# Kernel optimization log

Hardware: AMD Instinct MI355X
Metric: run time of the kernel (lower is better)

## Reference

```python
import jax, jax.numpy as jnp
import numpy as np

B, N, V = 8, 2000, 2000
K = 100            # local_size
EMB = 128          # ff_hidden_dim
PENALTY = -1e9
EPS = 1e-5         # InstanceNorm eps


def setup_inputs() -> dict:
    key = jax.random.key(0)
    ks = jax.random.split(key, 16)
    s = 0.02
    return {
        "dist": jax.random.uniform(ks[0], (B, N, V), dtype=jnp.float32),
        "theta": jax.random.normal(ks[1], (B, N, V), dtype=jnp.float32),
        "scale": jax.random.uniform(ks[2], (B, N, 1), dtype=jnp.float32),
        # Linear params stored [in, out]
        "w1": jax.random.normal(ks[3], (2 * K + 1, EMB), dtype=jnp.float32) * s,
        "b1": jnp.zeros((EMB,), jnp.float32),
        "w2": jax.random.normal(ks[4], (EMB, 2 * EMB), dtype=jnp.float32) * s,
        "b2": jnp.zeros((2 * EMB,), jnp.float32),
        "w3": jax.random.normal(ks[5], (2 * EMB, EMB), dtype=jnp.float32) * s,
        "b3": jnp.zeros((EMB,), jnp.float32),
        "w4": jax.random.normal(ks[6], (EMB, K), dtype=jnp.float32) * s,
        "b4": jnp.zeros((K,), jnp.float32),
        "gamma": jnp.ones((2 * EMB,), jnp.float32),   # InstanceNorm affine weight
        "beta": jnp.zeros((2 * EMB,), jnp.float32),   # InstanceNorm affine bias
    }


def reference(dist, theta, scale, w1, b1, w2, b2, w3, b3, w4, b4, gamma, beta):
    # --- topk smallest distances (ascending) + gather theta ---
    neg_vals, idx = jax.lax.top_k(-dist, K)          # [B,N,K]
    sorted_dist = -neg_vals                           # ascending k smallest
    sorted_dist = sorted_dist / jnp.max(sorted_dist, axis=-1, keepdims=True)
    sorted_theta = jnp.take_along_axis(theta, idx, axis=-1)  # [B,N,K]

    # --- small MLP with InstanceNorm over the node dim ---
    x_in = jnp.concatenate([sorted_dist, sorted_theta, scale], axis=-1)  # [B,N,2K+1]
    emb = jax.nn.relu(x_in @ w1 + b1)                 # [B,N,EMB]
    h = jax.nn.relu(emb @ w2 + b2)                    # [B,N,2*EMB]
    # InstanceNorm1d: normalize each channel over the length (node) dim, biased var
    mean = jnp.mean(h, axis=1, keepdims=True)
    var = jnp.var(h, axis=1, keepdims=True)
    h = (h - mean) * jax.lax.rsqrt(var + EPS) * gamma + beta
    emb = jax.nn.relu(h @ w3 + b3)                    # [B,N,EMB]
    out = (emb @ w4 + b4) - sorted_dist               # [B,N,K]

    # --- scatter into penalty-initialized matrix ---
    out_mat = jnp.full((B, N, V), PENALTY, dtype=dist.dtype)
    b_ix = jnp.arange(B)[:, None, None]
    n_ix = jnp.arange(N)[None, :, None]
    return out_mat.at[b_ix, n_ix, idx].set(out)
```

## Files before the change

### kernel.cpp

```cpp
#include <hip/hip_runtime.h>
#include <hip/hip_bf16.h>

#define BB 8
#define NN 2000
#define VV 2000
#define KK 100
#define EMB 128
#define PENALTY -1e9f
#define NBIN 512
#define BINSCALE 2048.0f
#define CAP 200
#define XPAD 224

typedef __attribute__((ext_vector_type(8))) short short8;
typedef __attribute__((ext_vector_type(4))) float f32x4;

__device__ __forceinline__ unsigned short bf16rne(float f) {
    unsigned u = __float_as_uint(f);
    u += 0x7FFF + ((u >> 16) & 1);
    return (unsigned short)(u >> 16);
}
__device__ __forceinline__ float bf2f(unsigned short s) {
    return __uint_as_float((unsigned)s << 16);
}

__global__ __launch_bounds__(256) void wpack_kernel(
    const float* __restrict__ w1, const float* __restrict__ w2,
    const float* __restrict__ w3, const float* __restrict__ w4,
    unsigned short* __restrict__ pw1, unsigned short* __restrict__ pw2,
    unsigned short* __restrict__ pw3, unsigned short* __restrict__ pw4)
{
    const int bt = blockIdx.x;
    const int t = threadIdx.x;
    for (int e = t; e < 512; e += 256) {
        int lane = e >> 3, j = e & 7;
        int kk = ((lane >> 4) << 3) + j;
        int nn = lane & 15;
        if (bt < 56) {
            int kt = bt >> 3, nt = bt & 7;
            int k = kt * 32 + kk, n = nt * 16 + nn;
            float f = (k < 201) ? w1[k * 128 + n] : 0.f;
            pw1[bt * 512 + e] = bf16rne(f);
        } else if (bt < 120) {
            int bb = bt - 56, kt = bb >> 4, nt = bb & 15;
            pw2[bb * 512 + e] = bf16rne(w2[(kt * 32 + kk) * 256 + nt * 16 + nn]);
        } else if (bt < 184) {
            int bb = bt - 120, kt = bb >> 3, nt = bb & 7;
            pw3[bb * 512 + e] = bf16rne(w3[(kt * 32 + kk) * 128 + nt * 16 + nn]);
        } else {
            int bb = bt - 184, kt = bb / 7, nt = bb % 7;
            int n = nt * 16 + nn;
            float f = (n < 100) ? w4[(kt * 32 + kk) * 100 + n] : 0.f;
            pw4[bb * 512 + e] = bf16rne(f);
        }
    }
}

__global__ __launch_bounds__(256) void topk_kernel(
    const float* __restrict__ dist, const float* __restrict__ theta,
    const float* __restrict__ scale,
    unsigned short* __restrict__ xin, float* __restrict__ sdist,
    int* __restrict__ idxb)
{
    __shared__ __align__(16) unsigned hist[NBIN];
    __shared__ unsigned long long comp[CAP];
    __shared__ unsigned wsum[4];
    __shared__ int sh_Bt, sh_m, sh_mult;
    __shared__ int sh_cnt, sh_ntie, sh_kth;
    __shared__ unsigned sh_pref;
    __shared__ int sh_tie[64];
    __shared__ float sh_Tf;

    const int row = blockIdx.x;
    const int t = threadIdx.x;
    const int lane = t & 63, wid = t >> 6;
    const float* drow = dist + (size_t)row * VV;

    unsigned kb[8];
    int bn[8];
    if (t < VV / 8) {
        const float4* d4 = (const float4*)drow;
        float4 a = d4[t * 2], b2 = d4[t * 2 + 1];
        float vv[8] = {a.x, a.y, a.z, a.w, b2.x, b2.y, b2.z, b2.w};
#pragma unroll
        for (int j = 0; j < 8; ++j) {
            kb[j] = __float_as_uint(vv[j]);
            int b = (int)(vv[j] * BINSCALE);
            bn[j] = b < 0 ? 0 : (b > NBIN - 1 ? NBIN - 1 : b);
        }
    } else {
#pragma unroll
        for (int j = 0; j < 8; ++j) { kb[j] = 0xFFFFFFFFu; bn[j] = NBIN - 1; }
    }

    hist[t] = 0u;
    hist[t + 256] = 0u;
    if (t == 0) { sh_cnt = 0; sh_ntie = 0; sh_mult = 1; sh_Bt = NBIN - 1; sh_m = 100000; }
    __syncthreads();
#pragma unroll
    for (int j = 0; j < 8; ++j)
        if (bn[j] < NBIN - 1) atomicAdd(&hist[bn[j]], 1u);
    __syncthreads();

    uint2 cc = *(const uint2*)&hist[2 * t];
    const unsigned c0 = cc.x, c1 = cc.y;
    const unsigned tot = c0 + c1;
    unsigned incl = tot;
#pragma unroll
    for (int off = 1; off < 64; off <<= 1) {
        unsigned v = __shfl_up(incl, (unsigned)off);
        if (lane >= off) incl += v;
    }
    if (lane == 63) wsum[wid] = incl;
    __syncthreads();
    unsigned woff = 0;
    for (int w = 0; w < wid; ++w) woff += wsum[w];
    const unsigned excl = woff + incl - tot;
    const unsigned run = excl + tot;

    { uint2 off2; off2.x = excl; off2.y = excl + c0; *(uint2*)&hist[2 * t] = off2; }
    if (excl < KK && excl + c0 >= KK) {
        sh_Bt = 2 * t; sh_m = (int)(excl + c0);
    } else if (t < 255 && excl + c0 < KK && run >= KK) {
        sh_Bt = 2 * t + 1; sh_m = (int)run;
    }
    __syncthreads();
    const int Bt = sh_Bt;
    const int m = sh_m;

    {
        int mx = 0;
        if (2 * t <= Bt) mx = (int)c0;
        if (2 * t + 1 <= Bt) mx = mx > (int)c1 ? mx : (int)c1;
        if (mx > 1) atomicMax(&sh_mult, mx);
    }

    if (m <= CAP) {
#pragma unroll
        for (int j = 0; j < 8; ++j) {
            if (bn[j] <= Bt) {
                int slot = (int)atomicAdd(&hist[bn[j]], 1u);
                comp[slot] = ((unsigned long long)kb[j] << 32) | (unsigned)(t * 8 + j);
            }
        }
        __syncthreads();
        const int passes = (sh_mult > 1) ? sh_mult + 1 : 0;
        for (int p = 0; p < passes; ++p) {
            int i = 2 * t + (p & 1);
            if (i + 1 < m) {
                unsigned long long a = comp[i], b2 = comp[i + 1];
                if (a > b2) { comp[i] = b2; comp[i + 1] = a; }
            }
            __syncthreads();
        }
        const float Tf = __uint_as_float((unsigned)(comp[KK - 1] >> 32));
        const float invT = 1.0f / Tf;
        const float* trow = theta + (size_t)row * VV;
        if (t < KK) {
            unsigned long long c = comp[t];
            unsigned kbits = (unsigned)(c >> 32);
            int id = (int)(c & 0xFFFFFFFFu);
            float nv = __uint_as_float(kbits) * invT;
            xin[(size_t)row * XPAD + t] = bf16rne(nv);
            xin[(size_t)row * XPAD + 100 + t] = bf16rne(trow[id]);
            sdist[(size_t)row * KK + t] = nv;
            idxb[(size_t)row * KK + t] = id;
        }
        if (t == 255) xin[(size_t)row * XPAD + 200] = bf16rne(scale[row]);
    } else {
#pragma unroll
        for (int j = 0; j < 8; ++j) {
            if (bn[j] < Bt) {
                int pos = atomicAdd(&sh_cnt, 1);
                if (pos < CAP)
                    comp[pos] = ((unsigned long long)kb[j] << 32) | (unsigned)(t * 8 + j);
            }
        }
        __syncthreads();
        int nless = sh_cnt;
        if (t == 0) { sh_pref = 0u; sh_kth = KK - nless; }
        __syncthreads();
        for (int p = 0; p < 4; ++p) {
            if (t < 256) hist[t] = 0u;
            __syncthreads();
            const int shift = 24 - 8 * p;
            const unsigned pref = sh_pref;
#pragma unroll
            for (int j = 0; j < 8; ++j) {
                if (bn[j] == Bt) {
                    unsigned k = kb[j];
                    bool ok = (p == 0) || ((k >> (shift + 8)) == pref);
                    if (ok) atomicAdd(&hist[(k >> shift) & 255u], 1u);
                }
            }
            __syncthreads();
            if (t == 0) {
                int kth = sh_kth;
                unsigned cum = 0;
                int b = 0;
                for (; b < 256; ++b) {
                    unsigned c = hist[b];
                    if (cum + c >= (unsigned)kth) break;
                    cum += c;
                }
                sh_pref = (pref << 8) | (unsigned)b;
                sh_kth = kth - (int)cum;
            }
            __syncthreads();
        }
        const unsigned T = sh_pref;
        const int need2 = sh_kth;
#pragma unroll
        for (int j = 0; j < 8; ++j) {
            if (bn[j] == Bt) {
                unsigned k = kb[j];
                if (k < T) {
                    int pos = atomicAdd(&sh_cnt, 1);
                    if (pos < CAP)
                        comp[pos] = ((unsigned long long)k << 32) | (unsigned)(t * 8 + j);
                } else if (k == T) {
                    int q = atomicAdd(&sh_ntie, 1);
                    if (q < 64) sh_tie[q] = t * 8 + j;
                }
            }
        }
        __syncthreads();
        if (t == 0) {
            int nl2 = sh_cnt;
            int nt = sh_ntie < 64 ? sh_ntie : 64;
            for (int i = 1; i < nt; ++i) {
                int v = sh_tie[i], j2 = i - 1;
                while (j2 >= 0 && sh_tie[j2] > v) { sh_tie[j2 + 1] = sh_tie[j2]; --j2; }
                sh_tie[j2 + 1] = v;
            }
            for (int i = 0; i < need2; ++i)
                comp[nl2 + i] = ((unsigned long long)T << 32) | (unsigned)sh_tie[i];
            sh_cnt = nl2 + need2;
        }
        __syncthreads();
        const int mm = sh_cnt;
        unsigned long long c = (t < mm) ? comp[t] : ~0ull;
        int rank = 0;
        if (t < mm) {
            for (int j = 0; j < mm; ++j) {
                unsigned long long cj = comp[j];
                rank += (cj < c) || (cj == c && j < t);
            }
            if (rank == KK - 1) sh_Tf = __uint_as_float((unsigned)(c >> 32));
        }
        __syncthreads();
        const float invT = 1.0f / sh_Tf;
        const float* trow = theta + (size_t)row * VV;
        if (t < mm && rank < KK) {
            unsigned kbits = (unsigned)(c >> 32);
            int id = (int)(c & 0xFFFFFFFFu);
            float nv = __uint_as_float(kbits) * invT;
            xin[(size_t)row * XPAD + rank] = bf16rne(nv);
            xin[(size_t)row * XPAD + 100 + rank] = bf16rne(trow[id]);
            sdist[(size_t)row * KK + rank] = nv;
            idxb[(size_t)row * KK + rank] = id;
        }
        if (t == 255) xin[(size_t)row * XPAD + 200] = bf16rne(scale[row]);
    }
}

__global__ __launch_bounds__(256) void fused12_mfma(
    const unsigned short* __restrict__ xin, const unsigned short* __restrict__ pw1,
    const float* __restrict__ b1, const unsigned short* __restrict__ pw2,
    const float* __restrict__ b2, unsigned short* __restrict__ h)
{
    __shared__ unsigned short c1s[64][136];
    const int t = threadIdx.x;
    const int w = t >> 6, l = t & 63;
    const int m0 = blockIdx.x * 64;
    const int lr = l & 15, lg = l >> 4;

    f32x4 acc[8] = {};
    const short8* arow = (const short8*)(xin + (size_t)(m0 + 16 * w + lr) * XPAD);
    const short8* pw1v = (const short8*)pw1;
#pragma unroll
    for (int kt = 0; kt < 7; ++kt) {
        short8 a = arow[kt * 4 + lg];
#pragma unroll
        for (int nt = 0; nt < 8; ++nt) {
            short8 b = pw1v[(kt * 8 + nt) * 64 + l];
            acc[nt] = __builtin_amdgcn_mfma_f32_16x16x32_bf16(a, b, acc[nt], 0, 0, 0);
        }
    }
#pragma unroll
    for (int nt = 0; nt < 8; ++nt) {
        int col = nt * 16 + lr;
        float bb = b1[col];
#pragma unroll
        for (int r = 0; r < 4; ++r) {
            float v = fmaxf(acc[nt][r] + bb, 0.f);
            c1s[16 * w + lg * 4 + r][col] = bf16rne(v);
        }
    }
    __syncthreads();

    f32x4 acc2[16] = {};
    const short8* pw2v = (const short8*)pw2;
#pragma unroll
    for (int kt = 0; kt < 4; ++kt) {
        short8 a = *(const short8*)&c1s[16 * w + lr][kt * 32 + lg * 8];
#pragma unroll
        for (int nt = 0; nt < 16; ++nt) {
            short8 b = pw2v[(kt * 16 + nt) * 64 + l];
            acc2[nt] = __builtin_amdgcn_mfma_f32_16x16x32_bf16(a, b, acc2[nt], 0, 0, 0);
        }
    }
#pragma unroll
    for (int nt = 0; nt < 16; ++nt) {
        int col = nt * 16 + lr;
        float bb = b2[col];
#pragma unroll
        for (int r = 0; r < 4; ++r) {
            float v = fmaxf(acc2[nt][r] + bb, 0.f);
            h[(size_t)(m0 + 16 * w + lg * 4 + r) * 256 + col] = bf16rne(v);
        }
    }
}

#define NCHUNK 25
#define CHUNK (NN / NCHUNK)

__global__ __launch_bounds__(256) void stats_partial(
    const unsigned short* __restrict__ h, float* __restrict__ part)
{
    const int b = blockIdx.x, ch = blockIdx.y, c = threadIdx.x;
    const unsigned short* base = h + ((size_t)b * NN + (size_t)ch * CHUNK) * 256 + c;
    float s = 0.f, s2 = 0.f;
    for (int n = 0; n < CHUNK; ++n) {
        float v = bf2f(base[(size_t)n * 256]);
        s += v;
        s2 += v * v;
    }
    size_t o = (((size_t)b * NCHUNK + ch) * 256 + c) * 2;
    part[o] = s;
    part[o + 1] = s2;
}

__global__ __launch_bounds__(256) void stats_final(
    const float* __restrict__ part, const float* __restrict__ gamma,
    const float* __restrict__ beta, float* __restrict__ scv,
    float* __restrict__ shv)
{
    const int b = blockIdx.x, c = threadIdx.x;
    float s = 0.f, s2 = 0.f;
    for (int ch = 0; ch < NCHUNK; ++ch) {
        size_t o = (((size_t)b * NCHUNK + ch) * 256 + c) * 2;
        s += part[o];
        s2 += part[o + 1];
    }
    const float inv = 1.0f / (float)NN;
    float mean = s * inv;
    float var = s2 * inv - mean * mean;
    float rs = rsqrtf(var + 1e-5f);
    float sc = gamma[c] * rs;
    scv[b * 256 + c] = sc;
    shv[b * 256 + c] = beta[c] - mean * sc;
}

__global__ __launch_bounds__(256) void fused34_mfma(
    const unsigned short* __restrict__ h, const unsigned short* __restrict__ pw3,
    const float* __restrict__ b3, const unsigned short* __restrict__ pw4,
    const float* __restrict__ b4, const float* __restrict__ scv,
    const float* __restrict__ shv, const float* __restrict__ sdist,
    const int* __restrict__ idxb, float* __restrict__ out)
{
    __shared__ unsigned short c1s[64][136];
    const int t = threadIdx.x;
    const int w = t >> 6, l = t & 63;
    const int m0 = blockIdx.x * 64;
    const int lr = l & 15, lg = l >> 4;

    {
        float4* o4 = (float4*)(out + (size_t)m0 * VV);
        const float4 pv = make_float4(PENALTY, PENALTY, PENALTY, PENALTY);
        for (int i = t; i < 64 * VV / 4; i += 256) o4[i] = pv;
    }

    const int myrow = m0 + 16 * w + lr;
    const int mybatch = myrow / NN;

    f32x4 acc[8] = {};
    const short8* hrow = (const short8*)(h + (size_t)myrow * 256);
    const short8* pw3v = (const short8*)pw3;
#pragma unroll
    for (int kt = 0; kt < 8; ++kt) {
        int k0 = kt * 32 + lg * 8;
        short8 hv = hrow[kt * 4 + lg];
        const float4* scp = (const float4*)(scv + mybatch * 256 + k0);
        const float4* shp = (const float4*)(shv + mybatch * 256 + k0);
        float4 sc0 = scp[0], sc1 = scp[1];
        float4 sh0 = shp[0], sh1 = shp[1];
        short8 a;
        a[0] = (short)bf16rne(fmaf(bf2f((unsigned short)hv[0]), sc0.x, sh0.x));
        a[1] = (short)bf16rne(fmaf(bf2f((unsigned short)hv[1]), sc0.y, sh0.y));
        a[2] = (short)bf16rne(fmaf(bf2f((unsigned short)hv[2]), sc0.z, sh0.z));
        a[3] = (short)bf16rne(fmaf(bf2f((unsigned short)hv[3]), sc0.w, sh0.w));
        a[4] = (short)bf16rne(fmaf(bf2f((unsigned short)hv[4]), sc1.x, sh1.x));
        a[5] = (short)bf16rne(fmaf(bf2f((unsigned short)hv[5]), sc1.y, sh1.y));
        a[6] = (short)bf16rne(fmaf(bf2f((unsigned short)hv[6]), sc1.z, sh1.z));
        a[7] = (short)bf16rne(fmaf(bf2f((unsigned short)hv[7]), sc1.w, sh1.w));
#pragma unroll
        for (int nt = 0; nt < 8; ++nt) {
            short8 b = pw3v[(kt * 8 + nt) * 64 + l];
            acc[nt] = __builtin_amdgcn_mfma_f32_16x16x32_bf16(a, b, acc[nt], 0, 0, 0);
        }
    }
#pragma unroll
    for (int nt = 0; nt < 8; ++nt) {
        int col = nt * 16 + lr;
        float bb = b3[col];
#pragma unroll
        for (int r = 0; r < 4; ++r) {
            float v = fmaxf(acc[nt][r] + bb, 0.f);
            c1s[16 * w + lg * 4 + r][col] = bf16rne(v);
        }
    }
    __syncthreads();

    f32x4 acc2[7] = {};
    const short8* pw4v = (const short8*)pw4;
#pragma unroll
    for (int kt = 0; kt < 4; ++kt) {
        short8 a = *(const short8*)&c1s[16 * w + lr][kt * 32 + lg * 8];
#pragma unroll
        for (int nt = 0; nt < 7; ++nt) {
            short8 b = pw4v[(kt * 7 + nt) * 64 + l];
            acc2[nt] = __builtin_amdgcn_mfma_f32_16x16x32_bf16(a, b, acc2[nt], 0, 0, 0);
        }
    }
#pragma unroll
    for (int nt = 0; nt < 7; ++nt) {
        int col = nt * 16 + lr;
        if (col < KK) {
            float bb = b4[col];
#pragma unroll
            for (int r = 0; r < 4; ++r) {
                int mrow = m0 + 16 * w + lg * 4 + r;
                float v = acc2[nt][r] + bb - sdist[(size_t)mrow * KK + col];
                int id = idxb[(size_t)mrow * KK + col];
                out[(size_t)mrow * VV + id] = v;
            }
        }
    }
}

extern "C" void kernel_launch(void* const* d_in, const int* in_sizes, int n_in,
                              void* d_out, int out_size, void* d_ws, size_t ws_size,
                              hipStream_t stream)
{
    const float* dist  = (const float*)d_in[0];
    const float* theta = (const float*)d_in[1];
    const float* scale = (const float*)d_in[2];
    const float* w1 = (const float*)d_in[3];
    const float* b1 = (const float*)d_in[4];
    const float* w2 = (const float*)d_in[5];
    const float* b2 = (const float*)d_in[6];
    const float* w3 = (const float*)d_in[7];
    const float* b3 = (const float*)d_in[8];
    const float* w4 = (const float*)d_in[9];
    const float* b4 = (const float*)d_in[10];
    const float* gamma = (const float*)d_in[11];
    const float* beta  = (const float*)d_in[12];
    float* out = (float*)d_out;

    const int M = BB * NN;

    char* p = (char*)d_ws;
    unsigned short* xin = (unsigned short*)p;       p += (size_t)M * XPAD * 2;
    unsigned short* h   = (unsigned short*)p;       p += (size_t)M * 256 * 2;
    float* sdist = (float*)p;                       p += (size_t)M * KK * 4;
    int*   idxb  = (int*)p;                         p += (size_t)M * KK * 4;
    float* part  = (float*)p;                       p += (size_t)BB * NCHUNK * 256 * 2 * 4;
    float* scv   = (float*)p;                       p += 8 * 256 * 4;
    float* shv   = (float*)p;                       p += 8 * 256 * 4;
    unsigned short* pw1 = (unsigned short*)p;       p += 56 * 512 * 2;
    unsigned short* pw2 = (unsigned short*)p;       p += 64 * 512 * 2;
    unsigned short* pw3 = (unsigned short*)p;       p += 64 * 512 * 2;
    unsigned short* pw4 = (unsigned short*)p;       p += 28 * 512 * 2;

    wpack_kernel<<<212, 256, 0, stream>>>(w1, w2, w3, w4, pw1, pw2, pw3, pw4);

    topk_kernel<<<M, 256, 0, stream>>>(dist, theta, scale, xin, sdist, idxb);

    fused12_mfma<<<M / 64, 256, 0, stream>>>(xin, pw1, b1, pw2, b2, h);

    stats_partial<<<dim3(BB, NCHUNK), 256, 0, stream>>>(h, part);
    stats_final<<<BB, 256, 0, stream>>>(part, gamma, beta, scv, shv);

    fused34_mfma<<<M / 64, 256, 0, stream>>>(h, pw3, b3, pw4, b4, scv, shv,
                                             sdist, idxb, out);
}
```

Baseline: 140.9 us.

## Move penalty fill into topk, rank-sort within bins, split theta gather out

Three changes. The penalty fill of the output moves from the final MLP kernel into the top-k kernel, where it can overlap with the dist loads that kernel is memory-bound on. The odd-even transposition sort over bins is replaced by a per-element rank count within each bin, followed by a scatter, which removes the sort's many barrier passes. The theta gather moves out of the top-k kernel into a separate gather kernel, which adds a launch and extra reads of idxb.

```diff
diff --git a/kernel.cpp b/kernel.cpp
--- a/kernel.cpp
+++ b/kernel.cpp
@@ -57,15 +57,15 @@
 }
 
 __global__ __launch_bounds__(256) void topk_kernel(
-    const float* __restrict__ dist, const float* __restrict__ theta,
-    const float* __restrict__ scale,
+    const float* __restrict__ dist, const float* __restrict__ scale,
     unsigned short* __restrict__ xin, float* __restrict__ sdist,
-    int* __restrict__ idxb)
+    int* __restrict__ idxb, float* __restrict__ out)
 {
     __shared__ __align__(16) unsigned hist[NBIN];
+    __shared__ __align__(16) unsigned binstart[NBIN];
     __shared__ unsigned long long comp[CAP];
     __shared__ unsigned wsum[4];
-    __shared__ int sh_Bt, sh_m, sh_mult;
+    __shared__ int sh_Bt, sh_m;
     __shared__ int sh_cnt, sh_ntie, sh_kth;
     __shared__ unsigned sh_pref;
     __shared__ int sh_tie[64];
@@ -76,11 +76,24 @@
     const int lane = t & 63, wid = t >> 6;
     const float* drow = dist + (size_t)row * VV;
 
+    float4 a, b2;
+    const bool live = (t < VV / 8);
+    if (live) {
+        const float4* d4 = (const float4*)drow;
+        a = d4[t * 2];
+        b2 = d4[t * 2 + 1];
+    }
+
+    {
+        float4* orow4 = (float4*)(out + (size_t)row * VV);
+        const float4 pv = make_float4(PENALTY, PENALTY, PENALTY, PENALTY);
+        orow4[t] = pv;
+        if (t + 256 < VV / 4) orow4[t + 256] = pv;
+    }
+
     unsigned kb[8];
     int bn[8];
-    if (t < VV / 8) {
-        const float4* d4 = (const float4*)drow;
-        float4 a = d4[t * 2], b2 = d4[t * 2 + 1];
+    if (live) {
         float vv[8] = {a.x, a.y, a.z, a.w, b2.x, b2.y, b2.z, b2.w};
 #pragma unroll
         for (int j = 0; j < 8; ++j) {
@@ -95,7 +108,7 @@
 
     hist[t] = 0u;
     hist[t + 256] = 0u;
-    if (t == 0) { sh_cnt = 0; sh_ntie = 0; sh_mult = 1; sh_Bt = NBIN - 1; sh_m = 100000; }
+    if (t == 0) { sh_cnt = 0; sh_ntie = 0; sh_Bt = NBIN - 1; sh_m = 100000; }
     __syncthreads();
 #pragma unroll
     for (int j = 0; j < 8; ++j)
@@ -118,7 +131,11 @@
     const unsigned excl = woff + incl - tot;
     const unsigned run = excl + tot;
 
-    { uint2 off2; off2.x = excl; off2.y = excl + c0; *(uint2*)&hist[2 * t] = off2; }
+    {
+        uint2 st; st.x = excl; st.y = excl + c0;
+        *(uint2*)&hist[2 * t] = st;
+        *(uint2*)&binstart[2 * t] = st;
+    }
     if (excl < KK && excl + c0 >= KK) {
         sh_Bt = 2 * t; sh_m = (int)(excl + c0);
     } else if (t < 255 && excl + c0 < KK && run >= KK) {
@@ -128,41 +145,44 @@
     const int Bt = sh_Bt;
     const int m = sh_m;
 
-    {
-        int mx = 0;
-        if (2 * t <= Bt) mx = (int)c0;
-        if (2 * t + 1 <= Bt) mx = mx > (int)c1 ? mx : (int)c1;
-        if (mx > 1) atomicMax(&sh_mult, mx);
-    }
-
     if (m <= CAP) {
+        bool win[8];
 #pragma unroll
         for (int j = 0; j < 8; ++j) {
-            if (bn[j] <= Bt) {
+            win[j] = (bn[j] <= Bt);
+            if (win[j]) {
                 int slot = (int)atomicAdd(&hist[bn[j]], 1u);
                 comp[slot] = ((unsigned long long)kb[j] << 32) | (unsigned)(t * 8 + j);
             }
         }
         __syncthreads();
-        const int passes = (sh_mult > 1) ? sh_mult + 1 : 0;
-        for (int p = 0; p < passes; ++p) {
-            int i = 2 * t + (p & 1);
-            if (i + 1 < m) {
-                unsigned long long a = comp[i], b2 = comp[i + 1];
-                if (a > b2) { comp[i] = b2; comp[i + 1] = a; }
-            }
-            __syncthreads();
-        }
+        int rk[8];
+#pragma unroll
+        for (int j = 0; j < 8; ++j) {
+            if (win[j]) {
+                unsigned long long key =
+                    ((unsigned long long)kb[j] << 32) | (unsigned)(t * 8 + j);
+                unsigned s0 = binstart[bn[j]];
+                unsigned e0 = hist[bn[j]];
+                int r = (int)s0;
+                for (unsigned s = s0; s < e0; ++s) r += (comp[s] < key);
+                rk[j] = r;
+            }
+        }
+        __syncthreads();
+#pragma unroll
+        for (int j = 0; j < 8; ++j)
+            if (win[j])
+                comp[rk[j]] = ((unsigned long long)kb[j] << 32) | (unsigned)(t * 8 + j);
+        __syncthreads();
         const float Tf = __uint_as_float((unsigned)(comp[KK - 1] >> 32));
         const float invT = 1.0f / Tf;
-        const float* trow = theta + (size_t)row * VV;
         if (t < KK) {
             unsigned long long c = comp[t];
             unsigned kbits = (unsigned)(c >> 32);
             int id = (int)(c & 0xFFFFFFFFu);
             float nv = __uint_as_float(kbits) * invT;
             xin[(size_t)row * XPAD + t] = bf16rne(nv);
-            xin[(size_t)row * XPAD + 100 + t] = bf16rne(trow[id]);
             sdist[(size_t)row * KK + t] = nv;
             idxb[(size_t)row * KK + t] = id;
         }
@@ -250,18 +270,28 @@
         }
         __syncthreads();
         const float invT = 1.0f / sh_Tf;
-        const float* trow = theta + (size_t)row * VV;
         if (t < mm && rank < KK) {
             unsigned kbits = (unsigned)(c >> 32);
             int id = (int)(c & 0xFFFFFFFFu);
             float nv = __uint_as_float(kbits) * invT;
             xin[(size_t)row * XPAD + rank] = bf16rne(nv);
-            xin[(size_t)row * XPAD + 100 + rank] = bf16rne(trow[id]);
             sdist[(size_t)row * KK + rank] = nv;
             idxb[(size_t)row * KK + rank] = id;
         }
         if (t == 255) xin[(size_t)row * XPAD + 200] = bf16rne(scale[row]);
     }
+}
+
+__global__ __launch_bounds__(256) void gather_kernel(
+    const float* __restrict__ theta, const int* __restrict__ idxb,
+    unsigned short* __restrict__ xin)
+{
+    const int i = blockIdx.x * 256 + threadIdx.x;
+    const int row = i / KK;
+    const int k = i - row * KK;
+    const int id = idxb[i];
+    float v = theta[(size_t)row * VV + id];
+    xin[(size_t)row * XPAD + 100 + k] = bf16rne(v);
 }
 
 __global__ __launch_bounds__(256) void fused12_mfma(
@@ -374,12 +404,6 @@
     const int w = t >> 6, l = t & 63;
     const int m0 = blockIdx.x * 64;
     const int lr = l & 15, lg = l >> 4;
-
-    {
-        float4* o4 = (float4*)(out + (size_t)m0 * VV);
-        const float4 pv = make_float4(PENALTY, PENALTY, PENALTY, PENALTY);
-        for (int i = t; i < 64 * VV / 4; i += 256) o4[i] = pv;
-    }
 
     const int myrow = m0 + 16 * w + lr;
     const int mybatch = myrow / NN;
@@ -485,7 +509,9 @@
 
     wpack_kernel<<<212, 256, 0, stream>>>(w1, w2, w3, w4, pw1, pw2, pw3, pw4);
 
-    topk_kernel<<<M, 256, 0, stream>>>(dist, theta, scale, xin, sdist, idxb);
+    topk_kernel<<<M, 256, 0, stream>>>(dist, scale, xin, sdist, idxb, out);
+
+    gather_kernel<<<(M * KK) / 256, 256, 0, stream>>>(theta, idxb, xin);
 
     fused12_mfma<<<M / 64, 256, 0, stream>>>(xin, pw1, b1, pw2, b2, h);
 
```

After: 144.8 us. 2.7% more time.

## Process one top-k row per wavefront and split theta gather into separate kernel

Applied to the files above, without the earlier changes.

The top-k kernel now gives each 64-lane wavefront its own row, with four rows per block. All block-wide __syncthreads are replaced by wave barriers and per-wave shared arrays. The odd-even transposition sort of candidates is replaced by a per-bin rank computation that scatters into a second buffer. The theta gather moves into a separate elementwise kernel to spread the random reads across more threads. The aim is to remove block synchronisation overhead and serial sort passes, at the cost of more shared memory per block, an extra launch, and a round-trip of idx through global memory.

```diff
diff --git a/kernel.cpp b/kernel.cpp
--- a/kernel.cpp
+++ b/kernel.cpp
@@ -15,6 +15,8 @@
 typedef __attribute__((ext_vector_type(8))) short short8;
 typedef __attribute__((ext_vector_type(4))) float f32x4;
 
+#define WB() __builtin_amdgcn_wave_barrier()
+
 __device__ __forceinline__ unsigned short bf16rne(float f) {
     unsigned u = __float_as_uint(f);
     u += 0x7FFF + ((u >> 16) & 1);
@@ -23,6 +25,14 @@
 __device__ __forceinline__ float bf2f(unsigned short s) {
     return __uint_as_float((unsigned)s << 16);
 }
+
+#define FORALL_VALS(BODY)                                                    \
+    _Pragma("unroll") for (int c = 0; c < 8; ++c) {                          \
+        { const float fv = v4[c].x; const int e = (c * 64 + lane) * 4 + 0; BODY } \
+        { const float fv = v4[c].y; const int e = (c * 64 + lane) * 4 + 1; BODY } \
+        { const float fv = v4[c].z; const int e = (c * 64 + lane) * 4 + 2; BODY } \
+        { const float fv = v4[c].w; const int e = (c * 64 + lane) * 4 + 3; BODY } \
+    }
 
 __global__ __launch_bounds__(256) void wpack_kernel(
     const float* __restrict__ w1, const float* __restrict__ w2,
@@ -57,211 +67,232 @@
 }
 
 __global__ __launch_bounds__(256) void topk_kernel(
-    const float* __restrict__ dist, const float* __restrict__ theta,
-    const float* __restrict__ scale,
+    const float* __restrict__ dist, const float* __restrict__ scale,
     unsigned short* __restrict__ xin, float* __restrict__ sdist,
     int* __restrict__ idxb)
 {
-    __shared__ __align__(16) unsigned hist[NBIN];
-    __shared__ unsigned long long comp[CAP];
-    __shared__ unsigned wsum[4];
-    __shared__ int sh_Bt, sh_m, sh_mult;
-    __shared__ int sh_cnt, sh_ntie, sh_kth;
-    __shared__ unsigned sh_pref;
-    __shared__ int sh_tie[64];
-    __shared__ float sh_Tf;
-
-    const int row = blockIdx.x;
+    __shared__ __align__(16) unsigned hist[4][NBIN];
+    __shared__ __align__(16) unsigned binstart[4][NBIN];
+    __shared__ unsigned long long comp[4][CAP];
+    __shared__ unsigned long long comp2[4][CAP];
+    __shared__ int sh_cnt[4], sh_ntie[4], sh_kth[4];
+    __shared__ unsigned sh_pref[4];
+    __shared__ int sh_tie[4][64];
+
     const int t = threadIdx.x;
-    const int lane = t & 63, wid = t >> 6;
-    const float* drow = dist + (size_t)row * VV;
-
-    unsigned kb[8];
-    int bn[8];
-    if (t < VV / 8) {
-        const float4* d4 = (const float4*)drow;
-        float4 a = d4[t * 2], b2 = d4[t * 2 + 1];
-        float vv[8] = {a.x, a.y, a.z, a.w, b2.x, b2.y, b2.z, b2.w};
-#pragma unroll
-        for (int j = 0; j < 8; ++j) {
-            kb[j] = __float_as_uint(vv[j]);
-            int b = (int)(vv[j] * BINSCALE);
-            bn[j] = b < 0 ? 0 : (b > NBIN - 1 ? NBIN - 1 : b);
-        }
-    } else {
-#pragma unroll
-        for (int j = 0; j < 8; ++j) { kb[j] = 0xFFFFFFFFu; bn[j] = NBIN - 1; }
-    }
-
-    hist[t] = 0u;
-    hist[t + 256] = 0u;
-    if (t == 0) { sh_cnt = 0; sh_ntie = 0; sh_mult = 1; sh_Bt = NBIN - 1; sh_m = 100000; }
-    __syncthreads();
-#pragma unroll
-    for (int j = 0; j < 8; ++j)
-        if (bn[j] < NBIN - 1) atomicAdd(&hist[bn[j]], 1u);
-    __syncthreads();
-
-    uint2 cc = *(const uint2*)&hist[2 * t];
-    const unsigned c0 = cc.x, c1 = cc.y;
-    const unsigned tot = c0 + c1;
+    const int w = t >> 6, lane = t & 63;
+    const int row = blockIdx.x * 4 + w;
+    const float4* d4 = (const float4*)(dist + (size_t)row * VV);
+
+    float4 v4[8];
+#pragma unroll
+    for (int c = 0; c < 7; ++c) v4[c] = d4[c * 64 + lane];
+    v4[7] = (lane < 52) ? d4[448 + lane] : make_float4(2.f, 2.f, 2.f, 2.f);
+
+    {
+        uint4 z = make_uint4(0u, 0u, 0u, 0u);
+        *(uint4*)&hist[w][lane * 8] = z;
+        *(uint4*)&hist[w][lane * 8 + 4] = z;
+    }
+    if (lane == 0) { sh_cnt[w] = 0; sh_ntie[w] = 0; }
+    WB();
+
+    FORALL_VALS({
+        int b = (int)(fv * BINSCALE);
+        b = b < 0 ? 0 : b;
+        if (b < NBIN - 1) atomicAdd(&hist[w][b], 1u);
+        (void)e;
+    });
+    WB();
+
+    uint4 h0 = *(const uint4*)&hist[w][lane * 8];
+    uint4 h1 = *(const uint4*)&hist[w][lane * 8 + 4];
+    unsigned c8[8] = {h0.x, h0.y, h0.z, h0.w, h1.x, h1.y, h1.z, h1.w};
+    unsigned tot = 0;
+#pragma unroll
+    for (int b = 0; b < 8; ++b) tot += c8[b];
     unsigned incl = tot;
 #pragma unroll
     for (int off = 1; off < 64; off <<= 1) {
         unsigned v = __shfl_up(incl, (unsigned)off);
         if (lane >= off) incl += v;
     }
-    if (lane == 63) wsum[wid] = incl;
-    __syncthreads();
-    unsigned woff = 0;
-    for (int w = 0; w < wid; ++w) woff += wsum[w];
-    const unsigned excl = woff + incl - tot;
-    const unsigned run = excl + tot;
-
-    { uint2 off2; off2.x = excl; off2.y = excl + c0; *(uint2*)&hist[2 * t] = off2; }
-    if (excl < KK && excl + c0 >= KK) {
-        sh_Bt = 2 * t; sh_m = (int)(excl + c0);
-    } else if (t < 255 && excl + c0 < KK && run >= KK) {
-        sh_Bt = 2 * t + 1; sh_m = (int)run;
-    }
-    __syncthreads();
-    const int Bt = sh_Bt;
-    const int m = sh_m;
-
+    const unsigned excl = incl - tot;
+
+    int myBt = -1, myM = 0;
     {
-        int mx = 0;
-        if (2 * t <= Bt) mx = (int)c0;
-        if (2 * t + 1 <= Bt) mx = mx > (int)c1 ? mx : (int)c1;
-        if (mx > 1) atomicMax(&sh_mult, mx);
+        unsigned runv = excl;
+        unsigned st[8];
+#pragma unroll
+        for (int b = 0; b < 8; ++b) {
+            st[b] = runv;
+            if (myBt < 0 && runv < KK && runv + c8[b] >= KK) {
+                myBt = lane * 8 + b;
+                myM = (int)(runv + c8[b]);
+            }
+            runv += c8[b];
+        }
+        uint4 s0 = make_uint4(st[0], st[1], st[2], st[3]);
+        uint4 s1 = make_uint4(st[4], st[5], st[6], st[7]);
+        *(uint4*)&hist[w][lane * 8] = s0;
+        *(uint4*)&hist[w][lane * 8 + 4] = s1;
+        *(uint4*)&binstart[w][lane * 8] = s0;
+        *(uint4*)&binstart[w][lane * 8 + 4] = s1;
+    }
+    WB();
+
+    unsigned long long bl = __ballot(myBt >= 0);
+    int Bt, m;
+    if (bl != 0ull) {
+        int src = __ffsll(bl) - 1;
+        Bt = __shfl(myBt, src);
+        m = __shfl(myM, src);
+    } else {
+        Bt = NBIN - 1;
+        m = 100000;
     }
 
     if (m <= CAP) {
-#pragma unroll
-        for (int j = 0; j < 8; ++j) {
-            if (bn[j] <= Bt) {
-                int slot = (int)atomicAdd(&hist[bn[j]], 1u);
-                comp[slot] = ((unsigned long long)kb[j] << 32) | (unsigned)(t * 8 + j);
-            }
-        }
-        __syncthreads();
-        const int passes = (sh_mult > 1) ? sh_mult + 1 : 0;
-        for (int p = 0; p < passes; ++p) {
-            int i = 2 * t + (p & 1);
-            if (i + 1 < m) {
-                unsigned long long a = comp[i], b2 = comp[i + 1];
-                if (a > b2) { comp[i] = b2; comp[i + 1] = a; }
-            }
-            __syncthreads();
-        }
-        const float Tf = __uint_as_float((unsigned)(comp[KK - 1] >> 32));
-        const float invT = 1.0f / Tf;
-        const float* trow = theta + (size_t)row * VV;
-        if (t < KK) {
-            unsigned long long c = comp[t];
-            unsigned kbits = (unsigned)(c >> 32);
-            int id = (int)(c & 0xFFFFFFFFu);
-            float nv = __uint_as_float(kbits) * invT;
-            xin[(size_t)row * XPAD + t] = bf16rne(nv);
-            xin[(size_t)row * XPAD + 100 + t] = bf16rne(trow[id]);
-            sdist[(size_t)row * KK + t] = nv;
-            idxb[(size_t)row * KK + t] = id;
-        }
-        if (t == 255) xin[(size_t)row * XPAD + 200] = bf16rne(scale[row]);
+        FORALL_VALS({
+            int b = (int)(fv * BINSCALE);
+            b = b < 0 ? 0 : (b > NBIN - 1 ? NBIN - 1 : b);
+            if (b <= Bt) {
+                int slot = (int)atomicAdd(&hist[w][b], 1u);
+                comp[w][slot] =
+                    ((unsigned long long)__float_as_uint(fv) << 32) | (unsigned)e;
+            }
+        });
+        WB();
+        FORALL_VALS({
+            int b = (int)(fv * BINSCALE);
+            b = b < 0 ? 0 : (b > NBIN - 1 ? NBIN - 1 : b);
+            if (b <= Bt) {
+                unsigned long long key =
+                    ((unsigned long long)__float_as_uint(fv) << 32) | (unsigned)e;
+                unsigned s0 = binstart[w][b];
+                unsigned e0 = hist[w][b];
+                int r = (int)s0;
+                for (unsigned s = s0; s < e0; ++s) r += (comp[w][s] < key);
+                comp2[w][r] = key;
+            }
+        });
     } else {
-#pragma unroll
-        for (int j = 0; j < 8; ++j) {
-            if (bn[j] < Bt) {
-                int pos = atomicAdd(&sh_cnt, 1);
+        FORALL_VALS({
+            int b = (int)(fv * BINSCALE);
+            b = b < 0 ? 0 : (b > NBIN - 1 ? NBIN - 1 : b);
+            if (b < Bt) {
+                int pos = atomicAdd(&sh_cnt[w], 1);
                 if (pos < CAP)
-                    comp[pos] = ((unsigned long long)kb[j] << 32) | (unsigned)(t * 8 + j);
-            }
-        }
-        __syncthreads();
-        int nless = sh_cnt;
-        if (t == 0) { sh_pref = 0u; sh_kth = KK - nless; }
-        __syncthreads();
+                    comp[w][pos] =
+                        ((unsigned long long)__float_as_uint(fv) << 32) | (unsigned)e;
+            }
+        });
+        WB();
+        int nless = sh_cnt[w];
+        if (lane == 0) { sh_pref[w] = 0u; sh_kth[w] = KK - nless; }
+        WB();
         for (int p = 0; p < 4; ++p) {
-            if (t < 256) hist[t] = 0u;
-            __syncthreads();
+            { uint4 z = make_uint4(0u, 0u, 0u, 0u); *(uint4*)&hist[w][lane * 4] = z; }
+            WB();
             const int shift = 24 - 8 * p;
-            const unsigned pref = sh_pref;
-#pragma unroll
-            for (int j = 0; j < 8; ++j) {
-                if (bn[j] == Bt) {
-                    unsigned k = kb[j];
+            const unsigned pref = sh_pref[w];
+            FORALL_VALS({
+                int b = (int)(fv * BINSCALE);
+                b = b < 0 ? 0 : (b > NBIN - 1 ? NBIN - 1 : b);
+                if (b == Bt) {
+                    unsigned k = __float_as_uint(fv);
                     bool ok = (p == 0) || ((k >> (shift + 8)) == pref);
-                    if (ok) atomicAdd(&hist[(k >> shift) & 255u], 1u);
+                    if (ok) atomicAdd(&hist[w][(k >> shift) & 255u], 1u);
                 }
-            }
-            __syncthreads();
-            if (t == 0) {
-                int kth = sh_kth;
+                (void)e;
+            });
+            WB();
+            if (lane == 0) {
+                int kth = sh_kth[w];
                 unsigned cum = 0;
                 int b = 0;
                 for (; b < 256; ++b) {
-                    unsigned c = hist[b];
-                    if (cum + c >= (unsigned)kth) break;
-                    cum += c;
+                    unsigned cc = hist[w][b];
+                    if (cum + cc >= (unsigned)kth) break;
+                    cum += cc;
                 }
-                sh_pref = (pref << 8) | (unsigned)b;
-                sh_kth = kth - (int)cum;
-            }
-            __syncthreads();
-        }
-        const unsigned T = sh_pref;
-        const int need2 = sh_kth;
-#pragma unroll
-        for (int j = 0; j < 8; ++j) {
-            if (bn[j] == Bt) {
-                unsigned k = kb[j];
+                sh_pref[w] = (pref << 8) | (unsigned)b;
+                sh_kth[w] = kth - (int)cum;
+            }
+            WB();
+        }
+        const unsigned T = sh_pref[w];
+        const int need2 = sh_kth[w];
+        FORALL_VALS({
+            int b = (int)(fv * BINSCALE);
+            b = b < 0 ? 0 : (b > NBIN - 1 ? NBIN - 1 : b);
+            if (b == Bt) {
+                unsigned k = __float_as_uint(fv);
                 if (k < T) {
-                    int pos = atomicAdd(&sh_cnt, 1);
+                    int pos = atomicAdd(&sh_cnt[w], 1);
                     if (pos < CAP)
-                        comp[pos] = ((unsigned long long)k << 32) | (unsigned)(t * 8 + j);
+                        comp[w][pos] = ((unsigned long long)k << 32) | (unsigned)e;
                 } else if (k == T) {
-                    int q = atomicAdd(&sh_ntie, 1);
-                    if (q < 64) sh_tie[q] = t * 8 + j;
+                    int q = atomicAdd(&sh_ntie[w], 1);
+                    if (q < 64) sh_tie[w][q] = e;
                 }
             }
-        }
-        __syncthreads();
-        if (t == 0) {
-            int nl2 = sh_cnt;
-            int nt = sh_ntie < 64 ? sh_ntie : 64;
+        });
+        WB();
+        if (lane == 0) {
+            int nl2 = sh_cnt[w];
+            int nt = sh_ntie[w] < 64 ? sh_ntie[w] : 64;
             for (int i = 1; i < nt; ++i) {
-                int v = sh_tie[i], j2 = i - 1;
-                while (j2 >= 0 && sh_tie[j2] > v) { sh_tie[j2 + 1] = sh_tie[j2]; --j2; }
-                sh_tie[j2 + 1] = v;
+                int v = sh_tie[w][i], j2 = i - 1;
+                while (j2 >= 0 && sh_tie[w][j2] > v) {
+                    sh_tie[w][j2 + 1] = sh_tie[w][j2];
+                    --j2;
+                }
+                sh_tie[w][j2 + 1] = v;
             }
             for (int i = 0; i < need2; ++i)
-                comp[nl2 + i] = ((unsigned long long)T << 32) | (unsigned)sh_tie[i];
-            sh_cnt = nl2 + need2;
-        }
-        __syncthreads();
-        const int mm = sh_cnt;
-        unsigned long long c = (t < mm) ? comp[t] : ~0ull;
-        int rank = 0;
-        if (t < mm) {
-            for (int j = 0; j < mm; ++j) {
-                unsigned long long cj = comp[j];
-                rank += (cj < c) || (cj == c && j < t);
-            }
-            if (rank == KK - 1) sh_Tf = __uint_as_float((unsigned)(c >> 32));
-        }
-        __syncthreads();
-        const float invT = 1.0f / sh_Tf;
-        const float* trow = theta + (size_t)row * VV;
-        if (t < mm && rank < KK) {
-            unsigned kbits = (unsigned)(c >> 32);
-            int id = (int)(c & 0xFFFFFFFFu);
-            float nv = __uint_as_float(kbits) * invT;
-            xin[(size_t)row * XPAD + rank] = bf16rne(nv);
-            xin[(size_t)row * XPAD + 100 + rank] = bf16rne(trow[id]);
-            sdist[(size_t)row * KK + rank] = nv;
-            idxb[(size_t)row * KK + rank] = id;
-        }
-        if (t == 255) xin[(size_t)row * XPAD + 200] = bf16rne(scale[row]);
-    }
+                comp[w][nl2 + i] =
+                    ((unsigned long long)T << 32) | (unsigned)sh_tie[w][i];
+            sh_cnt[w] = nl2 + need2;
+        }
+        WB();
+        const int mm = sh_cnt[w];
+        for (int o = lane; o < mm; o += 64) {
+            unsigned long long key = comp[w][o];
+            int r = 0;
+            for (int j2 = 0; j2 < mm; ++j2) {
+                unsigned long long cj = comp[w][j2];
+                r += (cj < key) || (cj == key && j2 < o);
+            }
+            if (r < CAP) comp2[w][r] = key;
+        }
+    }
+    WB();
+
+    const float Tf = __uint_as_float((unsigned)(comp2[w][KK - 1] >> 32));
+    const float invT = 1.0f / Tf;
+    for (int o = lane; o < KK; o += 64) {
+        unsigned long long c = comp2[w][o];
+        unsigned kbits = (unsigned)(c >> 32);
+        int id = (int)(c & 0xFFFFFFFFu);
+        float nv = __uint_as_float(kbits) * invT;
+        xin[(size_t)row * XPAD + o] = bf16rne(nv);
+        sdist[(size_t)row * KK + o] = nv;
+        idxb[(size_t)row * KK + o] = id;
+    }
+    if (lane == 0) xin[(size_t)row * XPAD + 200] = bf16rne(scale[row]);
+}
+
+__global__ __launch_bounds__(256) void gather_kernel(
+    const float* __restrict__ theta, const int* __restrict__ idxb,
+    unsigned short* __restrict__ xin)
+{
+    const int i = blockIdx.x * 256 + threadIdx.x;
+    const int row = i / KK;
+    const int k = i - row * KK;
+    const int id = idxb[i];
+    float v = theta[(size_t)row * VV + id];
+    xin[(size_t)row * XPAD + 100 + k] = bf16rne(v);
 }
 
 __global__ __launch_bounds__(256) void fused12_mfma(
@@ -485,7 +516,9 @@
 
     wpack_kernel<<<212, 256, 0, stream>>>(w1, w2, w3, w4, pw1, pw2, pw3, pw4);
 
-    topk_kernel<<<M, 256, 0, stream>>>(dist, theta, scale, xin, sdist, idxb);
+    topk_kernel<<<M / 4, 256, 0, stream>>>(dist, scale, xin, sdist, idxb);
+
+    gather_kernel<<<(M * KK) / 256, 256, 0, stream>>>(theta, idxb, xin);
 
     fused12_mfma<<<M / 64, 256, 0, stream>>>(xin, pw1, b1, pw2, b2, h);
 
```

Measured after the change: 173.2 us. 22.9% more time.
